# Kernel tuning notes

Hardware: AMD Instinct MI355X
Metric: run time of the kernel (lower is better)

## Reference

```python
import jax, jax.numpy as jnp
import numpy as np

D_MODEL = 1024

def setup_inputs() -> dict:
    key = jax.random.key(0)
    ks = jax.random.split(key, 7)
    B, S, D = 4, 2048, D_MODEL
    scale = 1.0 / np.sqrt(D)
    x = jax.random.normal(ks[0], (B, S, D), dtype=jnp.float32)
    Wq = jax.random.normal(ks[1], (D, D), dtype=jnp.float32) * scale
    bq = jax.random.normal(ks[2], (D,), dtype=jnp.float32) * 0.02
    Wk = jax.random.normal(ks[3], (D, D), dtype=jnp.float32) * scale
    bk = jax.random.normal(ks[4], (D,), dtype=jnp.float32) * 0.02
    Wv = jax.random.normal(ks[5], (D, D), dtype=jnp.float32) * scale
    bv = jax.random.normal(ks[6], (D,), dtype=jnp.float32) * 0.02
    return {"x": x, "Wq": Wq, "bq": bq, "Wk": Wk, "bk": bk, "Wv": Wv, "bv": bv}

def reference(x, Wq, bq, Wk, bk, Wv, bv):
    # x: [B, S, D]
    B, S, D = x.shape
    q = jnp.einsum('bsd,de->bse', x, Wq) + bq
    k = jnp.einsum('bsd,de,->bse'.replace(',->', '->'), x, Wk) + bk
    v = jnp.einsum('bsd,de->bse', x, Wv) + bv
    # scores: [B, S, S], scaled by 1/sqrt(d_model) with additive causal mask
    scores = jnp.einsum('bqd,bkd->bqk', q, k) / jnp.sqrt(jnp.float32(D))
    causal = jnp.triu(jnp.full((S, S), -jnp.inf, dtype=scores.dtype), k=1)
    probs = jax.nn.softmax(scores + causal, axis=-1)
    return jnp.einsum('bqk,bkd->bqd', probs, v)
```

## Files before the change

### kernel.cpp

```cpp
#include <hip/hip_runtime.h>
#include <hip/hip_bf16.h>

#define S_LEN 2048
#define DM 1024
#define NB 4

typedef __attribute__((ext_vector_type(8))) short short8;
typedef __attribute__((ext_vector_type(4))) short short4v;
typedef __attribute__((ext_vector_type(4))) float floatx4;

__device__ inline short f2bf(float f) {
    union { float f; unsigned u; } v; v.f = f;
    unsigned r = 0x7fffu + ((v.u >> 16) & 1u);
    return (short)((v.u + r) >> 16);
}

__device__ inline void load16(const short* g, short* l) {
    __builtin_amdgcn_global_load_lds(
        (const __attribute__((address_space(1))) void*)g,
        (__attribute__((address_space(3))) void*)l,
        16, 0, 0);
}

__device__ inline void gemm_core128(const short* __restrict__ A,
                                    const short* __restrict__ Bt,
                                    int lda, int ldb, int kLen,
                                    int m0, int n0, floatx4 acc[4][4],
                                    short* As, short* Bs) {
    const int tid  = threadIdx.x;
    const int lane = tid & 63;
    const int wave = tid >> 6;
    const int wr   = (wave >> 1) * 64;
    const int wc   = (wave & 1) * 64;
    const int quad = lane >> 4;
    const int l16  = lane & 15;

    const int srow = tid >> 4;
    const int g    = (tid & 15) ^ srow;
    const short* gA0 = A  + (size_t)(m0 + srow) * lda + g * 8;
    const short* gB0 = Bt + (size_t)(n0 + srow) * ldb + g * 8;
    short* lA0 = &As[wave * 512];
    short* lB0 = &Bs[wave * 512];

    const short* fa[4]; const short* fb[4];
#pragma unroll
    for (int h = 0; h < 4; h++) {
        int sw = ((h * 4 + quad) ^ l16) * 8;
        fa[h] = &As[(wr + l16) * 128 + sw];
        fb[h] = &Bs[(wc + l16) * 128 + sw];
    }

    for (int k0 = 0; k0 < kLen; k0 += 128) {
#pragma unroll
        for (int c = 0; c < 8; c++) load16(gA0 + (size_t)c * 16 * lda, lA0 + c * 2048);
#pragma unroll
        for (int c = 0; c < 8; c++) load16(gB0 + (size_t)c * 16 * ldb, lB0 + c * 2048);
        gA0 += 128; gB0 += 128;
        __syncthreads();

#pragma unroll
        for (int h = 0; h < 4; h++) {
            short8 af[4], bf[4];
#pragma unroll
            for (int t = 0; t < 4; t++) af[t] = *(const short8*)(fa[h] + t * 2048);
#pragma unroll
            for (int t = 0; t < 4; t++) bf[t] = *(const short8*)(fb[h] + t * 2048);
#pragma unroll
            for (int mt = 0; mt < 4; mt++)
#pragma unroll
                for (int nt = 0; nt < 4; nt++)
                    acc[mt][nt] = __builtin_amdgcn_mfma_f32_16x16x32_bf16(
                        af[mt], bf[nt], acc[mt][nt], 0, 0, 0);
        }
        __syncthreads();
    }
}

__global__ void prep(const float* __restrict__ x,
                     const float* __restrict__ Wq, const float* __restrict__ Wk,
                     const float* __restrict__ Wv,
                     short* __restrict__ xb, short* __restrict__ Wt) {
    __shared__ float t[64][65];
    int bid = blockIdx.x, tid = threadIdx.x;
    if (bid < 768) {
        int w = bid >> 8, tl = bid & 255;
        const float* W = (w == 0) ? Wq : (w == 1) ? Wk : Wv;
        short* out = Wt + (size_t)w * DM * DM;
        int bx = (tl & 15) * 64;
        int by = (tl >> 4) * 64;
        int tx = tid & 63, ty = tid >> 6;
        for (int r = ty; r < 64; r += 4)
            t[r][tx] = W[(size_t)(by + r) * DM + bx + tx];
        __syncthreads();
        for (int r = ty; r < 64; r += 4)
            out[(size_t)(bx + r) * DM + by + tx] = f2bf(t[tx][r]);
    } else {
        int i = (bid - 768) * 256 + tid;
        float4 v = ((const float4*)x)[i];
        short4v o;
        o.x = f2bf(v.x); o.y = f2bf(v.y); o.z = f2bf(v.z); o.w = f2bf(v.w);
        ((short4v*)xb)[i] = o;
    }
}

__global__ __launch_bounds__(256, 2)
void qkv_fused(const short* __restrict__ xb, const short* __restrict__ Wt,
               const float* __restrict__ bq, const float* __restrict__ bk,
               const float* __restrict__ bv,
               short* __restrict__ Qb, short* __restrict__ Kb,
               short* __restrict__ Vtb) {
    __shared__ short As[8192];
    __shared__ short Bs[3 * 8192];
    int n0 = blockIdx.x * 128;
    int m0 = blockIdx.y * 128;

    const int tid  = threadIdx.x;
    const int lane = tid & 63;
    const int wave = tid >> 6;
    const int wr   = (wave >> 1) * 64;
    const int wc   = (wave & 1) * 64;
    const int quad = lane >> 4;
    const int l16  = lane & 15;

    floatx4 acc[3][4][4];
#pragma unroll
    for (int w = 0; w < 3; w++)
#pragma unroll
        for (int i = 0; i < 4; i++)
#pragma unroll
            for (int j = 0; j < 4; j++) acc[w][i][j] = (floatx4){0.f, 0.f, 0.f, 0.f};

    const short* gA[4]; const short* gW[4];
    short* lA[4]; short* lB[4];
#pragma unroll
    for (int c = 0; c < 4; c++) {
        int idx = c * 256 + tid;
        int row = idx >> 3;
        int g = (idx & 7) ^ (row & 7);
        gA[c] = xb + (size_t)(m0 + row) * DM + g * 8;
        gW[c] = Wt + (size_t)(n0 + row) * DM + g * 8;
        int lbase = (c * 256 + wave * 64) * 8;
        lA[c] = &As[lbase];
        lB[c] = &Bs[lbase];
    }

    const short* fa[2]; const short* fb[2];
#pragma unroll
    for (int h = 0; h < 2; h++) {
        int sw = ((h * 4 + quad) ^ (l16 & 7)) * 8;
        fa[h] = &As[(wr + l16) * 64 + sw];
        fb[h] = &Bs[(wc + l16) * 64 + sw];
    }

    for (int k0 = 0; k0 < DM; k0 += 64) {
#pragma unroll
        for (int c = 0; c < 4; c++) load16(gA[c], lA[c]);
#pragma unroll
        for (int w = 0; w < 3; w++)
#pragma unroll
            for (int c = 0; c < 4; c++)
                load16(gW[c] + (size_t)w * DM * DM, lB[c] + w * 8192);
#pragma unroll
        for (int c = 0; c < 4; c++) { gA[c] += 64; gW[c] += 64; }
        __syncthreads();

#pragma unroll
        for (int h = 0; h < 2; h++) {
            short8 af[4];
#pragma unroll
            for (int t = 0; t < 4; t++) af[t] = *(const short8*)(fa[h] + t * 1024);
#pragma unroll
            for (int w = 0; w < 3; w++) {
                short8 bf[4];
#pragma unroll
                for (int t = 0; t < 4; t++)
                    bf[t] = *(const short8*)(fb[h] + w * 8192 + t * 1024);
#pragma unroll
                for (int mt = 0; mt < 4; mt++)
#pragma unroll
                    for (int nt = 0; nt < 4; nt++)
                        acc[w][mt][nt] = __builtin_amdgcn_mfma_f32_16x16x32_bf16(
                            af[mt], bf[nt], acc[w][mt][nt], 0, 0, 0);
            }
        }
        __syncthreads();
    }

#pragma unroll
    for (int w = 0; w < 2; w++) {
        short* out = w ? Kb : Qb;
        const float* bias = w ? bk : bq;
        float scale = w ? 1.0f : 0.03125f;
#pragma unroll
        for (int mt = 0; mt < 4; mt++)
#pragma unroll
            for (int nt = 0; nt < 4; nt++) {
                int col = n0 + wc + nt * 16 + l16;
                float bv_ = bias[col];
#pragma unroll
                for (int r = 0; r < 4; r++) {
                    int row = m0 + wr + mt * 16 + quad * 4 + r;
                    out[(size_t)row * DM + col] = f2bf((acc[w][mt][nt][r] + bv_) * scale);
                }
            }
    }

    {
        int b = m0 >> 11;
        int sbase = (m0 & 2047) + wr;
        float bvv[4];
#pragma unroll
        for (int nt = 0; nt < 4; nt++) bvv[nt] = bv[n0 + wc + nt * 16 + l16];
        short* buf = (wave & 1) ? Bs : As;
        short* vt = Vtb + ((size_t)b * DM + n0 + wc) * S_LEN;
#pragma unroll
        for (int p = 0; p < 2; p++) {
            __syncthreads();
            if ((wave >> 1) == p) {
#pragma unroll
                for (int mt = 0; mt < 4; mt++)
#pragma unroll
                    for (int nt = 0; nt < 4; nt++) {
                        int c = nt * 16 + l16;
                        short4v pk;
                        pk.x = f2bf(acc[2][mt][nt][0] + bvv[nt]);
                        pk.y = f2bf(acc[2][mt][nt][1] + bvv[nt]);
                        pk.z = f2bf(acc[2][mt][nt][2] + bvv[nt]);
                        pk.w = f2bf(acc[2][mt][nt][3] + bvv[nt]);
                        *(short4v*)&buf[c * 72 + mt * 16 + quad * 4] = pk;
                    }
                asm volatile("s_waitcnt lgkmcnt(0)" ::: "memory");
#pragma unroll
                for (int ps = 0; ps < 8; ps++) {
                    int dl = ps * 8 + (lane >> 3);
                    int sl = (lane & 7) * 8;
                    short8 row = *(short8*)&buf[dl * 72 + sl];
                    *(short8*)(vt + (size_t)dl * S_LEN + sbase + sl) = row;
                }
            }
        }
    }
}

__global__ __launch_bounds__(256, 2)
void score_gemm(const short* __restrict__ Qb, const short* __restrict__ Kb,
                short* __restrict__ P, float* __restrict__ denom) {
    __shared__ short As[128 * 64];
    __shared__ short Bs[256 * 64];

    const int bid = blockIdx.x;
    const int xcd = bid & 7;
    const int w   = bid >> 3;
    const int b   = w / 9;
    const int s   = w % 9;
    const int cx  = (xcd + 2) >> 1;
    const int it  = (s < cx) ? xcd : 15 - xcd;
    const int jt2 = (s < cx) ? s : s - cx;
    const int m0  = it * 128;
    const int n0  = jt2 * 256;

    const short* A  = Qb + (size_t)b * S_LEN * DM;
    const short* Bt = Kb + (size_t)b * S_LEN * DM;

    const int tid  = threadIdx.x;
    const int lane = tid & 63;
    const int wave = tid >> 6;
    const int wr   = (wave >> 1) * 64;
    const int wc   = (wave & 1) * 128;
    const int quad = lane >> 4;
    const int l16  = lane & 15;

    floatx4 acc[4][8];
#pragma unroll
    for (int i = 0; i < 4; i++)
#pragma unroll
        for (int j = 0; j < 8; j++) acc[i][j] = (floatx4){0.f, 0.f, 0.f, 0.f};

    const int g = (tid & 7) ^ ((tid >> 3) & 7);
    const short* gA0 = A  + (size_t)(m0 + (tid >> 3)) * DM + g * 8;
    const short* gB0 = Bt + (size_t)(n0 + (tid >> 3)) * DM + g * 8;
    short* lA0 = &As[wave * 512];
    short* lB0 = &Bs[wave * 512];

    const short* fa[2]; const short* fb[2];
#pragma unroll
    for (int h = 0; h < 2; h++) {
        int sw = ((h * 4 + quad) ^ (l16 & 7)) * 8;
        fa[h] = &As[(wr + l16) * 64 + sw];
        fb[h] = &Bs[(wc + l16) * 64 + sw];
    }

    for (int k0 = 0; k0 < DM; k0 += 64) {
#pragma unroll
        for (int c = 0; c < 4; c++) load16(gA0 + (size_t)c * 32 * DM, lA0 + c * 2048);
#pragma unroll
        for (int c = 0; c < 8; c++) load16(gB0 + (size_t)c * 32 * DM, lB0 + c * 2048);
        gA0 += 64; gB0 += 64;
        __syncthreads();

#pragma unroll
        for (int h = 0; h < 2; h++) {
            short8 af[4];
#pragma unroll
            for (int t = 0; t < 4; t++) af[t] = *(const short8*)(fa[h] + t * 1024);
            short8 bf[8];
#pragma unroll
            for (int t = 0; t < 8; t++) bf[t] = *(const short8*)(fb[h] + t * 1024);
#pragma unroll
            for (int mt = 0; mt < 4; mt++)
#pragma unroll
                for (int nt = 0; nt < 8; nt++)
                    acc[mt][nt] = __builtin_amdgcn_mfma_f32_16x16x32_bf16(
                        af[mt], bf[nt], acc[mt][nt], 0, 0, 0);
        }
        __syncthreads();
    }

    short* out = P + (size_t)b * S_LEN * S_LEN;
    float* dsum = denom + (size_t)b * S_LEN;
#pragma unroll
    for (int mt = 0; mt < 4; mt++) {
#pragma unroll
        for (int r = 0; r < 4; r++) {
            int row = m0 + wr + mt * 16 + quad * 4 + r;
            float psum = 0.f;
#pragma unroll
            for (int nt = 0; nt < 8; nt++) {
                int col = n0 + wc + nt * 16 + l16;
                float e = (col <= row) ? __expf(acc[mt][nt][r]) : 0.f;
                out[(size_t)row * S_LEN + col] = f2bf(e);
                psum += e;
            }
#pragma unroll
            for (int off = 8; off > 0; off >>= 1)
                psum += __shfl_down(psum, off, 16);
            if (l16 == 0) atomicAdd(&dsum[row], psum);
        }
    }
}

__global__ __launch_bounds__(256, 2)
void pv_gemm(const short* __restrict__ P, const short* __restrict__ Vtb,
             const float* __restrict__ denom, float* __restrict__ O) {
    __shared__ short As[16384];
    __shared__ short Bs[16384];
    int bid  = blockIdx.x;
    int xcd  = bid & 7;
    int wi   = bid >> 3;
    int b    = xcd >> 1;
    int dgrp = xcd & 1;
    int half = wi >> 5;
    int r    = (wi >> 2) & 7;
    int dl   = wi & 3;
    int it   = half ? r : 15 - r;
    int n0   = (dgrp * 4 + dl) * 128;
    int m0   = it * 128;
    int kLen = (it + 1) * 128;
    const short* A  = P   + (size_t)b * S_LEN * S_LEN;
    const short* Bt = Vtb + (size_t)b * DM * S_LEN;

    floatx4 acc[4][4];
#pragma unroll
    for (int i = 0; i < 4; i++)
#pragma unroll
        for (int j = 0; j < 4; j++) acc[i][j] = (floatx4){0.f, 0.f, 0.f, 0.f};

    gemm_core128(A, Bt, S_LEN, S_LEN, kLen, m0, n0, acc, As, Bs);

    float* out = O + (size_t)b * S_LEN * DM;
    const float* dsum = denom + (size_t)b * S_LEN;
    const int lane = threadIdx.x & 63, wave = threadIdx.x >> 6;
    const int wr = (wave >> 1) * 64, wc = (wave & 1) * 64;
    const int quad = lane >> 4, l16 = lane & 15;
#pragma unroll
    for (int mt = 0; mt < 4; mt++) {
#pragma unroll
        for (int r2 = 0; r2 < 4; r2++) {
            int row = m0 + wr + mt * 16 + quad * 4 + r2;
            float inv = 1.0f / dsum[row];
#pragma unroll
            for (int nt = 0; nt < 4; nt++) {
                int col = n0 + wc + nt * 16 + l16;
                out[(size_t)row * DM + col] = acc[mt][nt][r2] * inv;
            }
        }
    }
}

extern "C" void kernel_launch(void* const* d_in, const int* in_sizes, int n_in,
                              void* d_out, int out_size, void* d_ws, size_t ws_size,
                              hipStream_t stream) {
    const float* x  = (const float*)d_in[0];
    const float* Wq = (const float*)d_in[1];
    const float* bq = (const float*)d_in[2];
    const float* Wk = (const float*)d_in[3];
    const float* bk = (const float*)d_in[4];
    const float* Wv = (const float*)d_in[5];
    const float* bv = (const float*)d_in[6];
    float* out = (float*)d_out;

    char* ws = (char*)d_ws;
    const size_t MB = 1u << 20;
    short* xb    = (short*)(ws + 0);
    short* Wt    = (short*)(ws + 16 * MB);
    short* Qb    = (short*)(ws + 22 * MB);
    short* Kb    = (short*)(ws + 38 * MB);
    short* Vtb   = (short*)(ws + 54 * MB);
    short* P     = (short*)(ws + 70 * MB);
    float* denom = (float*)(ws + 102 * MB);

    hipMemsetAsync(denom, 0, (size_t)NB * S_LEN * sizeof(float), stream);
    prep<<<dim3(8960), dim3(256), 0, stream>>>(x, Wq, Wk, Wv, xb, Wt);
    qkv_fused<<<dim3(8, 64), dim3(256), 0, stream>>>(xb, Wt, bq, bk, bv, Qb, Kb, Vtb);
    score_gemm<<<dim3(288), dim3(256), 0, stream>>>(Qb, Kb, P, denom);
    pv_gemm<<<dim3(512), dim3(256), 0, stream>>>(P, Vtb, denom, out);
}
```

Before: 207.7 us.

## Widen QKV GEMM block to 256 rows and double-buffer weight tiles

```diff
diff --git a/kernel.cpp b/kernel.cpp
--- a/kernel.cpp
+++ b/kernel.cpp
@@ -103,16 +103,16 @@
     }
 }
 
-__global__ __launch_bounds__(256, 2)
-void qkv_fused(const short* __restrict__ xb, const short* __restrict__ Wt,
-               const float* __restrict__ bq, const float* __restrict__ bk,
-               const float* __restrict__ bv,
-               short* __restrict__ Qb, short* __restrict__ Kb,
-               short* __restrict__ Vtb) {
-    __shared__ short As[8192];
-    __shared__ short Bs[3 * 8192];
-    int n0 = blockIdx.x * 128;
-    int m0 = blockIdx.y * 128;
+__global__ __launch_bounds__(512, 2)
+void qkv_wide(const short* __restrict__ xb, const short* __restrict__ Wt,
+              const float* __restrict__ bq, const float* __restrict__ bk,
+              const float* __restrict__ bv,
+              short* __restrict__ Qb, short* __restrict__ Kb,
+              short* __restrict__ Vtb) {
+    extern __shared__ short lds[];
+
+    const int n0 = blockIdx.x * 128;
+    const int m0 = blockIdx.y * 256;
 
     const int tid  = threadIdx.x;
     const int lane = tid & 63;
@@ -130,40 +130,52 @@
 #pragma unroll
             for (int j = 0; j < 4; j++) acc[w][i][j] = (floatx4){0.f, 0.f, 0.f, 0.f};
 
-    const short* gA[4]; const short* gW[4];
-    short* lA[4]; short* lB[4];
+    const short* gA[4];
 #pragma unroll
     for (int c = 0; c < 4; c++) {
-        int idx = c * 256 + tid;
+        int idx = c * 512 + tid;
         int row = idx >> 3;
         int g = (idx & 7) ^ (row & 7);
         gA[c] = xb + (size_t)(m0 + row) * DM + g * 8;
-        gW[c] = Wt + (size_t)(n0 + row) * DM + g * 8;
-        int lbase = (c * 256 + wave * 64) * 8;
-        lA[c] = &As[lbase];
-        lB[c] = &Bs[lbase];
-    }
-
-    const short* fa[2]; const short* fb[2];
+    }
+    const short* gB[2];
+#pragma unroll
+    for (int c = 0; c < 2; c++) {
+        int idx = c * 512 + tid;
+        int row = idx >> 3;
+        int g = (idx & 7) ^ (row & 7);
+        gB[c] = Wt + (size_t)(n0 + row) * DM + g * 8;
+    }
+    short* lA  = lds + wave * 512;
+    short* lB0 = lds + 16384 + wave * 512;
+
+    const short* fa[2]; int fbo[2];
 #pragma unroll
     for (int h = 0; h < 2; h++) {
         int sw = ((h * 4 + quad) ^ (l16 & 7)) * 8;
-        fa[h] = &As[(wr + l16) * 64 + sw];
-        fb[h] = &Bs[(wc + l16) * 64 + sw];
-    }
-
-    for (int k0 = 0; k0 < DM; k0 += 64) {
-#pragma unroll
-        for (int c = 0; c < 4; c++) load16(gA[c], lA[c]);
-#pragma unroll
-        for (int w = 0; w < 3; w++)
-#pragma unroll
-            for (int c = 0; c < 4; c++)
-                load16(gW[c] + (size_t)w * DM * DM, lB[c] + w * 8192);
-#pragma unroll
-        for (int c = 0; c < 4; c++) { gA[c] += 64; gW[c] += 64; }
-        __syncthreads();
-
+        fa[h]  = &lds[(wr + l16) * 64 + sw];
+        fbo[h] = (wc + l16) * 64 + sw;
+    }
+    const short* Bbase = lds + 16384;
+
+#pragma unroll
+    for (int w = 0; w < 3; w++)
+#pragma unroll
+        for (int c = 0; c < 2; c++)
+            load16(gB[c] + (size_t)w * DM * DM, lB0 + w * 8192 + c * 4096);
+#pragma unroll
+    for (int c = 0; c < 4; c++) load16(gA[c], lA + c * 4096);
+#pragma unroll
+    for (int w = 0; w < 3; w++)
+#pragma unroll
+        for (int c = 0; c < 2; c++)
+            load16(gB[c] + (size_t)w * DM * DM + 64, lB0 + 24576 + w * 8192 + c * 4096);
+    asm volatile("s_waitcnt vmcnt(6)" ::: "memory");
+    __builtin_amdgcn_s_barrier();
+    __builtin_amdgcn_sched_barrier(0);
+
+    for (int k = 0; k < 16; k++) {
+        const short* Bcur = Bbase + (k & 1) * 24576;
 #pragma unroll
         for (int h = 0; h < 2; h++) {
             short8 af[4];
@@ -174,7 +186,7 @@
                 short8 bf[4];
 #pragma unroll
                 for (int t = 0; t < 4; t++)
-                    bf[t] = *(const short8*)(fb[h] + w * 8192 + t * 1024);
+                    bf[t] = *(const short8*)(Bcur + w * 8192 + fbo[h] + t * 1024);
 #pragma unroll
                 for (int mt = 0; mt < 4; mt++)
 #pragma unroll
@@ -183,7 +195,29 @@
                             af[mt], bf[nt], acc[w][mt][nt], 0, 0, 0);
             }
         }
-        __syncthreads();
+        if (k == 15) break;
+        __builtin_amdgcn_s_barrier();
+        __builtin_amdgcn_sched_barrier(0);
+        {
+            const int koA = (k + 1) * 64;
+#pragma unroll
+            for (int c = 0; c < 4; c++) load16(gA[c] + koA, lA + c * 4096);
+            if (k < 14) {
+                const size_t koB = (size_t)(k + 2) * 64;
+                short* dB = lds + 16384 + (k & 1) * 24576 + wave * 512;
+#pragma unroll
+                for (int w = 0; w < 3; w++)
+#pragma unroll
+                    for (int c = 0; c < 2; c++)
+                        load16(gB[c] + (size_t)w * DM * DM + koB,
+                               dB + w * 8192 + c * 4096);
+                asm volatile("s_waitcnt vmcnt(6)" ::: "memory");
+            } else {
+                asm volatile("s_waitcnt vmcnt(0)" ::: "memory");
+            }
+        }
+        __builtin_amdgcn_s_barrier();
+        __builtin_amdgcn_sched_barrier(0);
     }
 
 #pragma unroll
@@ -206,38 +240,33 @@
     }
 
     {
+        __syncthreads();
         int b = m0 >> 11;
         int sbase = (m0 & 2047) + wr;
         float bvv[4];
 #pragma unroll
         for (int nt = 0; nt < 4; nt++) bvv[nt] = bv[n0 + wc + nt * 16 + l16];
-        short* buf = (wave & 1) ? Bs : As;
+        short* buf = lds + wave * 4608;
         short* vt = Vtb + ((size_t)b * DM + n0 + wc) * S_LEN;
 #pragma unroll
-        for (int p = 0; p < 2; p++) {
-            __syncthreads();
-            if ((wave >> 1) == p) {
-#pragma unroll
-                for (int mt = 0; mt < 4; mt++)
-#pragma unroll
-                    for (int nt = 0; nt < 4; nt++) {
-                        int c = nt * 16 + l16;
-                        short4v pk;
-                        pk.x = f2bf(acc[2][mt][nt][0] + bvv[nt]);
-                        pk.y = f2bf(acc[2][mt][nt][1] + bvv[nt]);
-                        pk.z = f2bf(acc[2][mt][nt][2] + bvv[nt]);
-                        pk.w = f2bf(acc[2][mt][nt][3] + bvv[nt]);
-                        *(short4v*)&buf[c * 72 + mt * 16 + quad * 4] = pk;
-                    }
-                asm volatile("s_waitcnt lgkmcnt(0)" ::: "memory");
-#pragma unroll
-                for (int ps = 0; ps < 8; ps++) {
-                    int dl = ps * 8 + (lane >> 3);
-                    int sl = (lane & 7) * 8;
-                    short8 row = *(short8*)&buf[dl * 72 + sl];
-                    *(short8*)(vt + (size_t)dl * S_LEN + sbase + sl) = row;
-                }
-            }
+        for (int mt = 0; mt < 4; mt++)
+#pragma unroll
+            for (int nt = 0; nt < 4; nt++) {
+                int c = nt * 16 + l16;
+                short4v pk;
+                pk.x = f2bf(acc[2][mt][nt][0] + bvv[nt]);
+                pk.y = f2bf(acc[2][mt][nt][1] + bvv[nt]);
+                pk.z = f2bf(acc[2][mt][nt][2] + bvv[nt]);
+                pk.w = f2bf(acc[2][mt][nt][3] + bvv[nt]);
+                *(short4v*)&buf[c * 72 + mt * 16 + quad * 4] = pk;
+            }
+        asm volatile("s_waitcnt lgkmcnt(0)" ::: "memory");
+#pragma unroll
+        for (int ps = 0; ps < 8; ps++) {
+            int dl = ps * 8 + (lane >> 3);
+            int sl = (lane & 7) * 8;
+            short8 row = *(short8*)&buf[dl * 72 + sl];
+            *(short8*)(vt + (size_t)dl * S_LEN + sbase + sl) = row;
         }
     }
 }
@@ -409,9 +438,16 @@
     short* P     = (short*)(ws + 70 * MB);
     float* denom = (float*)(ws + 102 * MB);
 
+    static bool attr_set = false;
+    if (!attr_set) {
+        hipFuncSetAttribute(reinterpret_cast<const void*>(qkv_wide),
+                            hipFuncAttributeMaxDynamicSharedMemorySize, 131072);
+        attr_set = true;
+    }
+
     hipMemsetAsync(denom, 0, (size_t)NB * S_LEN * sizeof(float), stream);
     prep<<<dim3(8960), dim3(256), 0, stream>>>(x, Wq, Wk, Wv, xb, Wt);
-    qkv_fused<<<dim3(8, 64), dim3(256), 0, stream>>>(xb, Wt, bq, bk, bv, Qb, Kb, Vtb);
+    qkv_wide<<<dim3(8, 32), dim3(512), 131072, stream>>>(xb, Wt, bq, bk, bv, Qb, Kb, Vtb);
     score_gemm<<<dim3(288), dim3(256), 0, stream>>>(Qb, Kb, P, denom);
     pv_gemm<<<dim3(512), dim3(256), 0, stream>>>(P, Vtb, denom, out);
 }
```

Result: slower. 220.2 us (+6.0%).

## Double-buffer K tile in score_gemm to overlap global loads with MFMA

Applied to the files above, without the earlier changes.

```diff
diff --git a/kernel.cpp b/kernel.cpp
--- a/kernel.cpp
+++ b/kernel.cpp
@@ -245,8 +245,7 @@
 __global__ __launch_bounds__(256, 2)
 void score_gemm(const short* __restrict__ Qb, const short* __restrict__ Kb,
                 short* __restrict__ P, float* __restrict__ denom) {
-    __shared__ short As[128 * 64];
-    __shared__ short Bs[256 * 64];
+    extern __shared__ short lds[];
 
     const int bid = blockIdx.x;
     const int xcd = bid & 7;
@@ -279,25 +278,29 @@
     const int g = (tid & 7) ^ ((tid >> 3) & 7);
     const short* gA0 = A  + (size_t)(m0 + (tid >> 3)) * DM + g * 8;
     const short* gB0 = Bt + (size_t)(n0 + (tid >> 3)) * DM + g * 8;
-    short* lA0 = &As[wave * 512];
-    short* lB0 = &Bs[wave * 512];
-
-    const short* fa[2]; const short* fb[2];
+    short* lA = lds + wave * 512;
+    short* lB = lds + 8192 + wave * 512;
+
+    const short* fa[2]; int fbo[2];
 #pragma unroll
     for (int h = 0; h < 2; h++) {
         int sw = ((h * 4 + quad) ^ (l16 & 7)) * 8;
-        fa[h] = &As[(wr + l16) * 64 + sw];
-        fb[h] = &Bs[(wc + l16) * 64 + sw];
-    }
-
-    for (int k0 = 0; k0 < DM; k0 += 64) {
-#pragma unroll
-        for (int c = 0; c < 4; c++) load16(gA0 + (size_t)c * 32 * DM, lA0 + c * 2048);
-#pragma unroll
-        for (int c = 0; c < 8; c++) load16(gB0 + (size_t)c * 32 * DM, lB0 + c * 2048);
-        gA0 += 64; gB0 += 64;
-        __syncthreads();
-
+        fa[h]  = &lds[(wr + l16) * 64 + sw];
+        fbo[h] = 8192 + (wc + l16) * 64 + sw;
+    }
+
+#pragma unroll
+    for (int c = 0; c < 4; c++) load16(gA0 + (size_t)c * 32 * DM, lA + c * 2048);
+#pragma unroll
+    for (int c = 0; c < 8; c++) load16(gB0 + (size_t)c * 32 * DM, lB + c * 2048);
+#pragma unroll
+    for (int c = 0; c < 8; c++) load16(gB0 + 64 + (size_t)c * 32 * DM, lB + 16384 + c * 2048);
+    asm volatile("s_waitcnt vmcnt(8)" ::: "memory");
+    __builtin_amdgcn_s_barrier();
+    __builtin_amdgcn_sched_barrier(0);
+
+    for (int k = 0; k < 16; k++) {
+        const int bo = (k & 1) * 16384;
 #pragma unroll
         for (int h = 0; h < 2; h++) {
             short8 af[4];
@@ -305,7 +308,8 @@
             for (int t = 0; t < 4; t++) af[t] = *(const short8*)(fa[h] + t * 1024);
             short8 bf[8];
 #pragma unroll
-            for (int t = 0; t < 8; t++) bf[t] = *(const short8*)(fb[h] + t * 1024);
+            for (int t = 0; t < 8; t++)
+                bf[t] = *(const short8*)(lds + fbo[h] + bo + t * 1024);
 #pragma unroll
             for (int mt = 0; mt < 4; mt++)
 #pragma unroll
@@ -313,7 +317,26 @@
                     acc[mt][nt] = __builtin_amdgcn_mfma_f32_16x16x32_bf16(
                         af[mt], bf[nt], acc[mt][nt], 0, 0, 0);
         }
-        __syncthreads();
+        if (k == 15) break;
+        __builtin_amdgcn_s_barrier();
+        __builtin_amdgcn_sched_barrier(0);
+        {
+            const int koA = (k + 1) * 64;
+#pragma unroll
+            for (int c = 0; c < 4; c++)
+                load16(gA0 + koA + (size_t)c * 32 * DM, lA + c * 2048);
+            if (k < 14) {
+                const int koB = (k + 2) * 64;
+#pragma unroll
+                for (int c = 0; c < 8; c++)
+                    load16(gB0 + koB + (size_t)c * 32 * DM, lB + bo + c * 2048);
+                asm volatile("s_waitcnt vmcnt(8)" ::: "memory");
+            } else {
+                asm volatile("s_waitcnt vmcnt(0)" ::: "memory");
+            }
+        }
+        __builtin_amdgcn_s_barrier();
+        __builtin_amdgcn_sched_barrier(0);
     }
 
     short* out = P + (size_t)b * S_LEN * S_LEN;
@@ -409,9 +432,16 @@
     short* P     = (short*)(ws + 70 * MB);
     float* denom = (float*)(ws + 102 * MB);
 
+    static bool attr_set = false;
+    if (!attr_set) {
+        hipFuncSetAttribute(reinterpret_cast<const void*>(score_gemm),
+                            hipFuncAttributeMaxDynamicSharedMemorySize, 81920);
+        attr_set = true;
+    }
+
     hipMemsetAsync(denom, 0, (size_t)NB * S_LEN * sizeof(float), stream);
     prep<<<dim3(8960), dim3(256), 0, stream>>>(x, Wq, Wk, Wv, xb, Wt);
     qkv_fused<<<dim3(8, 64), dim3(256), 0, stream>>>(xb, Wt, bq, bk, bv, Qb, Kb, Vtb);
-    score_gemm<<<dim3(288), dim3(256), 0, stream>>>(Qb, Kb, P, denom);
+    score_gemm<<<dim3(288), dim3(256), 81920, stream>>>(Qb, Kb, P, denom);
     pv_gemm<<<dim3(512), dim3(256), 0, stream>>>(P, Vtb, denom, out);
 }
```

Result: no change. 208.8 us (+0.5%).
